# Optimization experiments

Hardware: AMD Instinct MI355X
Metric: run time of the kernel (lower is better)

Reference implementation:

```python
import jax, jax.numpy as jnp
import numpy as np

N = 50000        # nodes
E = 800000       # edges
IN_FEAT = 128
OUT_FEAT = 64
HEADS = 4
NUM_CLASSES = 40
NEG_SLOPE = 0.2  # DGL GATConv default


def setup_inputs() -> dict:
    key = jax.random.key(0)
    ks = jax.random.split(key, 12)
    x = jax.random.normal(ks[0], (N, IN_FEAT), dtype=jnp.float32)
    src = jax.random.randint(ks[1], (E,), 0, N, dtype=jnp.int32)
    dst = jax.random.randint(ks[2], (E,), 0, N, dtype=jnp.int32)
    # layer 1 params: fc W1 [in, H*D], attn_l/attn_r [H, D], bias [H*D]
    s1 = 1.0 / np.sqrt(IN_FEAT)
    W1 = jax.random.normal(ks[3], (IN_FEAT, HEADS * OUT_FEAT), dtype=jnp.float32) * s1
    al1 = jax.random.normal(ks[4], (HEADS, OUT_FEAT), dtype=jnp.float32) * 0.1
    ar1 = jax.random.normal(ks[5], (HEADS, OUT_FEAT), dtype=jnp.float32) * 0.1
    b1 = jnp.zeros((HEADS * OUT_FEAT,), dtype=jnp.float32)
    # layer 2 params: fc W2 [H*D, C], attn [1, C], bias [C]
    hid = HEADS * OUT_FEAT
    s2 = 1.0 / np.sqrt(hid)
    W2 = jax.random.normal(ks[6], (hid, NUM_CLASSES), dtype=jnp.float32) * s2
    al2 = jax.random.normal(ks[7], (1, NUM_CLASSES), dtype=jnp.float32) * 0.1
    ar2 = jax.random.normal(ks[8], (1, NUM_CLASSES), dtype=jnp.float32) * 0.1
    b2 = jnp.zeros((NUM_CLASSES,), dtype=jnp.float32)
    return {"x": x, "src": src, "dst": dst,
            "W1": W1, "al1": al1, "ar1": ar1, "b1": b1,
            "W2": W2, "al2": al2, "ar2": ar2, "b2": b2}


def gat_layer(x, W, al, ar, bias, src, dst, heads, out_feat):
    n = x.shape[0]
    h = (x @ W).reshape(n, heads, out_feat)            # [N,H,D]
    el = jnp.sum(h * al[None], axis=-1)                # [N,H]
    er = jnp.sum(h * ar[None], axis=-1)                # [N,H]
    e = el[src] + er[dst]                              # [E,H]
    e = jnp.where(e > 0, e, NEG_SLOPE * e)             # LeakyReLU
    # segment softmax over edges sharing the same destination
    emax = jax.ops.segment_max(e, dst, num_segments=n)           # [N,H]
    emax = jnp.where(jnp.isfinite(emax), emax, 0.0)              # isolated nodes
    ee = jnp.exp(e - emax[dst])                                  # [E,H]
    denom = jax.ops.segment_sum(ee, dst, num_segments=n)         # [N,H]
    denom = jnp.where(denom > 0, denom, 1.0)
    alpha = ee / denom[dst]                                      # [E,H]
    msg = h[src] * alpha[:, :, None]                             # [E,H,D]
    out = jax.ops.segment_sum(msg, dst, num_segments=n)          # [N,H,D]
    return out + bias.reshape(1, heads, out_feat)


def reference(x, src, dst, W1, al1, ar1, b1, W2, al2, ar2, b2):
    h = gat_layer(x, W1, al1, ar1, b1, src, dst, HEADS, OUT_FEAT)  # [N,H,D]
    h = h.reshape(h.shape[0], HEADS * OUT_FEAT)
    h = jax.nn.elu(h)
    h = gat_layer(h, W2, al2, ar2, b2, src, dst, 1, NUM_CLASSES)   # [N,1,C]
    return jnp.squeeze(h, axis=1)                                   # [N,C]
```

## Files before the change

kernel.cpp:

```cpp
#include <hip/hip_runtime.h>

#define NN 50000
#define NE 800000
#define HID 256
#define NCLS 40

typedef short bf16x8 __attribute__((ext_vector_type(8)));
typedef float f32x4 __attribute__((ext_vector_type(4)));

__device__ inline unsigned short f2bf(float f) {
    unsigned int u = __float_as_uint(f);
    return (unsigned short)((u + 0x7FFFu + ((u >> 16) & 1u)) >> 16);
}
__device__ inline unsigned int pack2bf(float a, float b) {
    return (unsigned int)f2bf(a) | ((unsigned int)f2bf(b) << 16);
}
__device__ inline float2 bf2x(unsigned int u) {
    return make_float2(__uint_as_float(u << 16), __uint_as_float(u & 0xFFFF0000u));
}

__global__ void k_count(const int* __restrict__ dst, int* __restrict__ counts) {
    int e = blockIdx.x * 256 + threadIdx.x;
    if (e < NE) atomicAdd(&counts[dst[e]], 1);
}

__global__ void k_scanA(const int* __restrict__ counts, int* __restrict__ indptr,
                        int* __restrict__ bsum) {
    __shared__ int sh[256];
    int t = threadIdx.x;
    int idx = blockIdx.x * 256 + t;
    int c = idx < NN ? counts[idx] : 0;
    sh[t] = c;
    __syncthreads();
    for (int off = 1; off < 256; off <<= 1) {
        int v = (t >= off) ? sh[t - off] : 0;
        __syncthreads();
        sh[t] += v;
        __syncthreads();
    }
    if (idx < NN) indptr[idx] = sh[t] - c;
    if (t == 255) bsum[blockIdx.x] = sh[255];
}

__global__ void k_scanB(int* __restrict__ bsum, int nb) {
    __shared__ int sh[256];
    int t = threadIdx.x;
    int c = t < nb ? bsum[t] : 0;
    sh[t] = c;
    __syncthreads();
    for (int off = 1; off < 256; off <<= 1) {
        int v = (t >= off) ? sh[t - off] : 0;
        __syncthreads();
        sh[t] += v;
        __syncthreads();
    }
    if (t < nb) bsum[t] = sh[t] - c;
}

__global__ void k_scanC(int* __restrict__ indptr, const int* __restrict__ bsum,
                        int* __restrict__ fill) {
    int idx = blockIdx.x * 256 + threadIdx.x;
    if (idx < NN) {
        indptr[idx] += bsum[idx >> 8];
        fill[idx] = 0;
    }
    if (idx == 0) indptr[NN] = NE;
}

__global__ void k_scatterw(const int* __restrict__ src, const int* __restrict__ dst,
                           const int* __restrict__ indptr, int* __restrict__ fill,
                           const float* __restrict__ el1, const float* __restrict__ er1,
                           int* __restrict__ srcs, float4* __restrict__ w4) {
    int e = blockIdx.x * 256 + threadIdx.x;
    if (e < NE) {
        int d = dst[e];
        int s = src[e];
        int pos = atomicAdd(&fill[d], 1);
        int j = indptr[d] + pos;
        srcs[j] = s;
        float4 ls = *(const float4*)&el1[(size_t)s * 4];
        float4 rd = *(const float4*)&er1[(size_t)d * 4];
        float e0 = ls.x + rd.x, e1 = ls.y + rd.y, e2 = ls.z + rd.z, e3 = ls.w + rd.w;
        e0 = e0 > 0.f ? e0 : 0.2f * e0;
        e1 = e1 > 0.f ? e1 : 0.2f * e1;
        e2 = e2 > 0.f ? e2 : 0.2f * e2;
        e3 = e3 > 0.f ? e3 : 0.2f * e3;
        w4[j] = make_float4(__expf(e0), __expf(e1), __expf(e2), __expf(e3));
    }
}

__global__ void k_prep(const float* __restrict__ W1, const float* __restrict__ al,
                       const float* __restrict__ ar, const float* __restrict__ W2,
                       float* __restrict__ wel, float* __restrict__ wer,
                       unsigned short* __restrict__ W1Tb,
                       unsigned short* __restrict__ W2Tb) {
    int gid = blockIdx.x * 256 + threadIdx.x;
    int nth = gridDim.x * 256;
    const int TOT = 512 + 32768 + 48 * 256;
    for (int i = gid; i < TOT; i += nth) {
        if (i < 512) {
            int k = i >> 2, h = i & 3;
            float a = 0.f, b = 0.f;
            for (int dd = 0; dd < 64; ++dd) {
                float w = W1[k * 256 + h * 64 + dd];
                a = fmaf(w, al[h * 64 + dd], a);
                b = fmaf(w, ar[h * 64 + dd], b);
            }
            wel[i] = a;
            wer[i] = b;
        } else if (i < 512 + 32768) {
            int j = i - 512;
            int col = j >> 7, k = j & 127;
            W1Tb[j] = f2bf(W1[k * 256 + col]);
        } else {
            int j = i - 512 - 32768;
            int col = j >> 8, kk = j & 255;
            W2Tb[j] = (col < NCLS) ? f2bf(W2[kk * 40 + col]) : (unsigned short)0;
        }
    }
}

__global__ void k_elr1x(const float* __restrict__ x, const float* __restrict__ wel,
                        const float* __restrict__ wer, float* __restrict__ el1,
                        float* __restrict__ er1, unsigned short* __restrict__ xb) {
    __shared__ float xs[64 * 129];
    __shared__ float wels[512], wers[512];
    int t = threadIdx.x;
    int n0 = blockIdx.x * 64;
    wels[t] = wel[t]; wels[256 + t] = wel[256 + t];
    wers[t] = wer[t]; wers[256 + t] = wer[256 + t];
    for (int i = 0; i < 8; ++i) {
        int f = i * 256 + t;
        int row = f >> 5;
        int col4 = (f & 31) * 4;
        float4 v = make_float4(0.f, 0.f, 0.f, 0.f);
        if (n0 + row < NN) v = ((const float4*)x)[(size_t)n0 * 32 + f];
        xs[row * 129 + col4 + 0] = v.x;
        xs[row * 129 + col4 + 1] = v.y;
        xs[row * 129 + col4 + 2] = v.z;
        xs[row * 129 + col4 + 3] = v.w;
    }
    __syncthreads();
    int node = t & 63;
    int h = t >> 6;
    float a = 0.f, b = 0.f;
    for (int k = 0; k < 128; ++k) {
        float xv = xs[node * 129 + k];
        a = fmaf(xv, wels[k * 4 + h], a);
        b = fmaf(xv, wers[k * 4 + h], b);
    }
    if (n0 + node < NN) {
        el1[(size_t)(n0 + node) * 4 + h] = a;
        er1[(size_t)(n0 + node) * 4 + h] = b;
    }
    for (int i = 0; i < 4; ++i) {
        int g = (i * 256 + t) * 8;
        int row = g >> 7, col = g & 127;
        if (n0 + row < NN) {
            ushort4 lo, hi;
            lo.x = f2bf(xs[row * 129 + col + 0]);
            lo.y = f2bf(xs[row * 129 + col + 1]);
            lo.z = f2bf(xs[row * 129 + col + 2]);
            lo.w = f2bf(xs[row * 129 + col + 3]);
            hi.x = f2bf(xs[row * 129 + col + 4]);
            hi.y = f2bf(xs[row * 129 + col + 5]);
            hi.z = f2bf(xs[row * 129 + col + 6]);
            hi.w = f2bf(xs[row * 129 + col + 7]);
            *(ushort4*)&xb[(size_t)(n0 + row) * 128 + col] = lo;
            *(ushort4*)&xb[(size_t)(n0 + row) * 128 + col + 4] = hi;
        }
    }
}

#define XG_STRIDE 260
#define FMA8(AC0, AC1, AC2, AC3, WQ, XV) \
    AC0.x = fmaf(WQ.x, XV.x, AC0.x); AC0.y = fmaf(WQ.x, XV.y, AC0.y); \
    AC1.x = fmaf(WQ.y, XV.x, AC1.x); AC1.y = fmaf(WQ.y, XV.y, AC1.y); \
    AC2.x = fmaf(WQ.z, XV.x, AC2.x); AC2.y = fmaf(WQ.z, XV.y, AC2.y); \
    AC3.x = fmaf(WQ.w, XV.x, AC3.x); AC3.y = fmaf(WQ.w, XV.y, AC3.y);

__global__ void k_agg1m(const unsigned int* __restrict__ xb32,
                        const float4* __restrict__ w4,
                        const int* __restrict__ indptr, const int* __restrict__ srcs,
                        const unsigned short* __restrict__ W1Tb,
                        const float* __restrict__ b1,
                        unsigned short* __restrict__ elu1) {
    __shared__ unsigned int xg[16 * XG_STRIDE];
    __shared__ int   si[8][64];
    __shared__ float4 sw[8][64];
    int t = threadIdx.x;
    int wv = t >> 6, l = t & 63;
    int n0 = blockIdx.x * 16;
    int d0 = n0 + wv * 4;
    int ip[5];
#pragma unroll
    for (int q = 0; q < 5; ++q) ip[q] = indptr[d0 + q];
    int w2 = wv * 2;
#pragma unroll
    for (int p = 0; p < 2; ++p) {
        int begA = ip[2 * p + 0], endA = ip[2 * p + 1];
        int begB = ip[2 * p + 1], endB = ip[2 * p + 2];
        int degA = endA - begA, degB = endB - begB;
        int sA = 0, sB = 0;
        float4 wA = make_float4(0.f, 0.f, 0.f, 0.f);
        float4 wB = make_float4(0.f, 0.f, 0.f, 0.f);
        if (l < degA) { sA = srcs[begA + l]; wA = w4[begA + l]; }
        if (l < degB) { sB = srcs[begB + l]; wB = w4[begB + l]; }
        si[w2 + 0][l] = sA; sw[w2 + 0][l] = wA;
        si[w2 + 1][l] = sB; sw[w2 + 1][l] = wB;
        float2 aA0 = {0,0}, aA1 = {0,0}, aA2 = {0,0}, aA3 = {0,0};
        float2 aB0 = {0,0}, aB1 = {0,0}, aB2 = {0,0}, aB3 = {0,0};
        int capA = degA < 64 ? degA : 64;
        int capB = degB < 64 ? degB : 64;
        int mcap = capA > capB ? capA : capB;
        for (int e = 0; e < mcap; e += 8) {
            unsigned int uA[8], uB[8];
            bool doA = e < capA, doB = e < capB;
            if (doA) {
#pragma unroll
                for (int q = 0; q < 8; ++q)
                    uA[q] = xb32[(size_t)si[w2][e + q] * 64 + l];
            }
            if (doB) {
#pragma unroll
                for (int q = 0; q < 8; ++q)
                    uB[q] = xb32[(size_t)si[w2 + 1][e + q] * 64 + l];
            }
            if (doA) {
#pragma unroll
                for (int q = 0; q < 8; ++q) {
                    float4 wq = sw[w2][e + q];
                    float2 xv = bf2x(uA[q]);
                    FMA8(aA0, aA1, aA2, aA3, wq, xv)
                }
            }
            if (doB) {
#pragma unroll
                for (int q = 0; q < 8; ++q) {
                    float4 wq = sw[w2 + 1][e + q];
                    float2 xv = bf2x(uB[q]);
                    FMA8(aB0, aB1, aB2, aB3, wq, xv)
                }
            }
        }
        for (int j = begA + 64; j < endA; ++j) {
            float4 wq = w4[j];
            float2 xv = bf2x(xb32[(size_t)srcs[j] * 64 + l]);
            FMA8(aA0, aA1, aA2, aA3, wq, xv)
        }
        for (int j = begB + 64; j < endB; ++j) {
            float4 wq = w4[j];
            float2 xv = bf2x(xb32[(size_t)srcs[j] * 64 + l]);
            FMA8(aB0, aB1, aB2, aB3, wq, xv)
        }
        float dA0 = wA.x, dA1 = wA.y, dA2 = wA.z, dA3 = wA.w;
        float dB0 = wB.x, dB1 = wB.y, dB2 = wB.z, dB3 = wB.w;
        for (int j = begA + 64 + l; j < endA; j += 64) {
            float4 wt = w4[j];
            dA0 += wt.x; dA1 += wt.y; dA2 += wt.z; dA3 += wt.w;
        }
        for (int j = begB + 64 + l; j < endB; j += 64) {
            float4 wt = w4[j];
            dB0 += wt.x; dB1 += wt.y; dB2 += wt.z; dB3 += wt.w;
        }
#pragma unroll
        for (int off = 32; off > 0; off >>= 1) {
            dA0 += __shfl_xor(dA0, off); dA1 += __shfl_xor(dA1, off);
            dA2 += __shfl_xor(dA2, off); dA3 += __shfl_xor(dA3, off);
            dB0 += __shfl_xor(dB0, off); dB1 += __shfl_xor(dB1, off);
            dB2 += __shfl_xor(dB2, off); dB3 += __shfl_xor(dB3, off);
        }
        float iA0 = dA0 > 0.f ? 1.f / dA0 : 0.f;
        float iA1 = dA1 > 0.f ? 1.f / dA1 : 0.f;
        float iA2 = dA2 > 0.f ? 1.f / dA2 : 0.f;
        float iA3 = dA3 > 0.f ? 1.f / dA3 : 0.f;
        float iB0 = dB0 > 0.f ? 1.f / dB0 : 0.f;
        float iB1 = dB1 > 0.f ? 1.f / dB1 : 0.f;
        float iB2 = dB2 > 0.f ? 1.f / dB2 : 0.f;
        float iB3 = dB3 > 0.f ? 1.f / dB3 : 0.f;
        unsigned int* xgA = &xg[(wv * 4 + 2 * p + 0) * XG_STRIDE];
        xgA[0 * 64 + l] = pack2bf(aA0.x * iA0, aA0.y * iA0);
        xgA[1 * 64 + l] = pack2bf(aA1.x * iA1, aA1.y * iA1);
        xgA[2 * 64 + l] = pack2bf(aA2.x * iA2, aA2.y * iA2);
        xgA[3 * 64 + l] = pack2bf(aA3.x * iA3, aA3.y * iA3);
        unsigned int* xgB = &xg[(wv * 4 + 2 * p + 1) * XG_STRIDE];
        xgB[0 * 64 + l] = pack2bf(aB0.x * iB0, aB0.y * iB0);
        xgB[1 * 64 + l] = pack2bf(aB1.x * iB1, aB1.y * iB1);
        xgB[2 * 64 + l] = pack2bf(aB2.x * iB2, aB2.y * iB2);
        xgB[3 * 64 + l] = pack2bf(aB3.x * iB3, aB3.y * iB3);
    }
    __syncthreads();
    int lrow = l & 15, lk = l >> 4;
    f32x4 acc[4] = {};
#pragma unroll
    for (int kt = 0; kt < 4; ++kt) {
        bf16x8 av = *(const bf16x8*)&xg[lrow * XG_STRIDE + wv * 64 + kt * 16 + lk * 4];
#pragma unroll
        for (int nt = 0; nt < 4; ++nt) {
            int col = wv * 64 + nt * 16 + lrow;
            bf16x8 bv = *(const bf16x8*)&W1Tb[(size_t)col * 128 + kt * 32 + lk * 8];
            acc[nt] = __builtin_amdgcn_mfma_f32_16x16x32_bf16(av, bv, acc[nt], 0, 0, 0);
        }
    }
#pragma unroll
    for (int nt = 0; nt < 4; ++nt) {
        int col = wv * 64 + nt * 16 + lrow;
        float bv1 = b1[col];
#pragma unroll
        for (int r = 0; r < 4; ++r) {
            int row = n0 + lk * 4 + r;
            float o = acc[nt][r] + bv1;
            o = o > 0.f ? o : (__expf(o) - 1.f);
            elu1[(size_t)row * 256 + col] = f2bf(o);
        }
    }
}

__global__ void k_mfma2(const unsigned short* __restrict__ elu1,
                        const unsigned short* __restrict__ W2Tb,
                        const float* __restrict__ al2, const float* __restrict__ ar2,
                        unsigned short* __restrict__ h2b, float* __restrict__ el2,
                        float* __restrict__ er2) {
    int t = threadIdx.x;
    int wv = t >> 6, l = t & 63;
    int lrow = l & 15, lk = l >> 4;
    int n0 = blockIdx.x * 64 + wv * 16;
    int arow = n0 + lrow;
    if (arow >= NN) arow = NN - 1;
    f32x4 acc[3] = {};
#pragma unroll
    for (int kt = 0; kt < 8; ++kt) {
        int kofs = kt * 32 + lk * 8;
        bf16x8 av = *(const bf16x8*)&elu1[(size_t)arow * 256 + kofs];
#pragma unroll
        for (int nt = 0; nt < 3; ++nt) {
            bf16x8 bv = *(const bf16x8*)&W2Tb[(size_t)(nt * 16 + lrow) * 256 + kofs];
            acc[nt] = __builtin_amdgcn_mfma_f32_16x16x32_bf16(av, bv, acc[nt], 0, 0, 0);
        }
    }
    float alc[3], arc[3];
#pragma unroll
    for (int nt = 0; nt < 3; ++nt) {
        int col = nt * 16 + lrow;
        alc[nt] = col < NCLS ? al2[col] : 0.f;
        arc[nt] = col < NCLS ? ar2[col] : 0.f;
    }
#pragma unroll
    for (int r = 0; r < 4; ++r) {
        int row = n0 + lk * 4 + r;
        float pa = 0.f, pb = 0.f;
#pragma unroll
        for (int nt = 0; nt < 3; ++nt) {
            float v = acc[nt][r];
            pa = fmaf(v, alc[nt], pa);
            pb = fmaf(v, arc[nt], pb);
            int col = nt * 16 + lrow;
            if (row < NN && col < NCLS) h2b[(size_t)row * NCLS + col] = f2bf(v);
        }
#pragma unroll
        for (int off = 1; off < 16; off <<= 1) {
            pa += __shfl_xor(pa, off);
            pb += __shfl_xor(pb, off);
        }
        if (lrow == 0 && row < NN) {
            el2[row] = pa;
            er2[row] = pb;
        }
    }
}

__global__ void k_agg2(const unsigned int* __restrict__ h2b32,
                       const float* __restrict__ el2,
                       const float* __restrict__ er2, const float* __restrict__ b2,
                       const int* __restrict__ indptr, const int* __restrict__ srcs,
                       float* __restrict__ out) {
    __shared__ int   si[4][64];
    __shared__ float sw[4][64];
    int t = threadIdx.x;
    int wv = t >> 6, l = t & 63;
    int d = blockIdx.x * 4 + wv;
    int beg = indptr[d], end = indptr[d + 1];
    int deg = end - beg;
    float rd = er2[d];
    int s_l = 0;
    float w = 0.f;
    if (l < deg) {
        s_l = srcs[beg + l];
        float e = el2[s_l] + rd;
        e = e > 0.f ? e : 0.2f * e;
        w = __expf(e);
    }
    si[wv][l] = s_l;
    sw[wv][l] = w;
    float den = w;
    for (int j = beg + 64 + l; j < end; j += 64) {
        float e = el2[srcs[j]] + rd;
        e = e > 0.f ? e : 0.2f * e;
        den += __expf(e);
    }
    int half = l >> 5, il = l & 31;
    bool act = il < 20;
    float2 acc = {0.f, 0.f};
    int dege = deg < 64 ? deg : 64;
    for (int e = 0; e < dege; e += 8) {
        int ixs[4];
        float ws_[4];
        unsigned int us[4];
#pragma unroll
        for (int q = 0; q < 4; ++q) {
            int idx = e + 2 * q + half;
            ixs[q] = si[wv][idx];
            ws_[q] = sw[wv][idx];
        }
#pragma unroll
        for (int q = 0; q < 4; ++q)
            us[q] = act ? h2b32[(size_t)ixs[q] * 20 + il] : 0u;
#pragma unroll
        for (int q = 0; q < 4; ++q) {
            float2 xv = bf2x(us[q]);
            acc.x = fmaf(ws_[q], xv.x, acc.x);
            acc.y = fmaf(ws_[q], xv.y, acc.y);
        }
    }
    for (int j = beg + 64; j < end; ++j) {
        int s = srcs[j];
        float e = el2[s] + rd;
        e = e > 0.f ? e : 0.2f * e;
        float ww = (half == 0) ? __expf(e) : 0.f;
        unsigned int u = act ? h2b32[(size_t)s * 20 + il] : 0u;
        float2 xv = bf2x(u);
        acc.x = fmaf(ww, xv.x, acc.x);
        acc.y = fmaf(ww, xv.y, acc.y);
    }
#pragma unroll
    for (int off = 32; off > 0; off >>= 1) den += __shfl_xor(den, off);
    float inv = den > 0.f ? 1.f / den : 0.f;
    acc.x += __shfl_xor(acc.x, 32);
    acc.y += __shfl_xor(acc.y, 32);
    if (half == 0 && act) {
        float2 bb = *(const float2*)&b2[2 * il];
        *(float2*)&out[(size_t)d * NCLS + 2 * il] =
            make_float2(fmaf(acc.x, inv, bb.x), fmaf(acc.y, inv, bb.y));
    }
}

extern "C" void kernel_launch(void* const* d_in, const int* in_sizes, int n_in,
                              void* d_out, int out_size, void* d_ws, size_t ws_size,
                              hipStream_t stream) {
    const float* x   = (const float*)d_in[0];
    const int*   src = (const int*)d_in[1];
    const int*   dst = (const int*)d_in[2];
    const float* W1  = (const float*)d_in[3];
    const float* al1 = (const float*)d_in[4];
    const float* ar1 = (const float*)d_in[5];
    const float* b1  = (const float*)d_in[6];
    const float* W2  = (const float*)d_in[7];
    const float* al2 = (const float*)d_in[8];
    const float* ar2 = (const float*)d_in[9];
    const float* b2  = (const float*)d_in[10];
    float* out = (float*)d_out;

    float* ws = (float*)d_ws;
    size_t off = 0;
    unsigned short* elu1  = (unsigned short*)(ws + off); off += (size_t)NN * 128;
    unsigned short* xb    = (unsigned short*)(ws + off); off += (size_t)NN * 64;
    unsigned short* h2b   = (unsigned short*)(ws + off); off += (size_t)NN * 20;
    float* el1  = ws + off; off += (size_t)NN * 4;
    float* er1  = ws + off; off += (size_t)NN * 4;
    float* el2  = ws + off; off += NN;
    float* er2  = ws + off; off += NN;
    float* wel  = ws + off; off += 512;
    float* wer  = ws + off; off += 512;
    unsigned short* w1tb = (unsigned short*)(ws + off); off += 16384;
    unsigned short* w2tb = (unsigned short*)(ws + off); off += 48 * 128;
    float* w4   = ws + off; off += (size_t)NE * 4;
    int* counts = (int*)(ws + off);
    int* indptr = counts + NN;
    int* fill   = indptr + NN + 1;
    int* srcs   = fill + NN;
    int* bsum   = srcs + NE;

    const int NB = (NN + 255) / 256;

    hipMemsetAsync(counts, 0, NN * sizeof(int), stream);

    k_count<<<(NE + 255) / 256, 256, 0, stream>>>(dst, counts);
    k_scanA<<<NB, 256, 0, stream>>>(counts, indptr, bsum);
    k_scanB<<<1, 256, 0, stream>>>(bsum, NB);
    k_scanC<<<NB, 256, 0, stream>>>(indptr, bsum, fill);

    k_prep<<<48, 256, 0, stream>>>(W1, al1, ar1, W2, wel, wer, w1tb, w2tb);
    k_elr1x<<<(NN + 63) / 64, 256, 0, stream>>>(x, wel, wer, el1, er1, xb);
    k_scatterw<<<(NE + 255) / 256, 256, 0, stream>>>(src, dst, indptr, fill,
                                                     el1, er1, srcs, (float4*)w4);
    k_agg1m<<<NN / 16, 256, 0, stream>>>((const unsigned int*)xb, (const float4*)w4,
                                         indptr, srcs, w1tb, b1, elu1);

    k_mfma2<<<(NN + 63) / 64, 256, 0, stream>>>(elu1, w2tb, al2, ar2, h2b, el2, er2);
    k_agg2<<<NN / 4, 256, 0, stream>>>((const unsigned int*)h2b, el2, er2, b2,
                                       indptr, srcs, out);
}
```

Before: 215.4 us.

## Fuse layer-2 projection into layer-1 aggregation and give each agg2 wave two nodes

Layer 1's ELU output is now staged in shared memory (reusing the edge-staging pool) and the W2 projection plus el2/er2 attention terms are computed in the same kernel. This removes the k_mfma2 launch and the 25.6 MB bf16 elu1 round trip through global memory. k_agg2 is also changed so each wave handles two destination nodes, halving the block count and interleaving the two gathers to raise memory-level parallelism. The cost is extra shared-memory syncs and a layer-2 MFMA that runs on only 3 of 4 waves in the fused kernel.

```diff
diff --git a/kernel.cpp b/kernel.cpp
--- a/kernel.cpp
+++ b/kernel.cpp
@@ -173,6 +173,7 @@
 }
 
 #define XG_STRIDE 260
+#define EB_STRIDE 264
 #define FMA8(AC0, AC1, AC2, AC3, WQ, XV) \
     AC0.x = fmaf(WQ.x, XV.x, AC0.x); AC0.y = fmaf(WQ.x, XV.y, AC0.y); \
     AC1.x = fmaf(WQ.y, XV.x, AC1.x); AC1.y = fmaf(WQ.y, XV.y, AC1.y); \
@@ -183,11 +184,18 @@
                         const float4* __restrict__ w4,
                         const int* __restrict__ indptr, const int* __restrict__ srcs,
                         const unsigned short* __restrict__ W1Tb,
+                        const unsigned short* __restrict__ W2Tb,
                         const float* __restrict__ b1,
-                        unsigned short* __restrict__ elu1) {
+                        const float* __restrict__ al2, const float* __restrict__ ar2,
+                        unsigned short* __restrict__ h2b,
+                        float* __restrict__ el2, float* __restrict__ er2) {
     __shared__ unsigned int xg[16 * XG_STRIDE];
-    __shared__ int   si[8][64];
-    __shared__ float4 sw[8][64];
+    __shared__ __align__(16) unsigned char pool[10496];
+    float4 (*sw)[64] = (float4(*)[64])pool;
+    int (*si)[64] = (int(*)[64])(pool + 8192);
+    unsigned short* eb = (unsigned short*)pool;
+    float* pel = (float*)(pool + 8448);
+    float* per_ = (float*)(pool + 8640);
     int t = threadIdx.x;
     int wv = t >> 6, l = t & 63;
     int n0 = blockIdx.x * 16;
@@ -291,81 +299,64 @@
     }
     __syncthreads();
     int lrow = l & 15, lk = l >> 4;
-    f32x4 acc[4] = {};
-#pragma unroll
-    for (int kt = 0; kt < 4; ++kt) {
-        bf16x8 av = *(const bf16x8*)&xg[lrow * XG_STRIDE + wv * 64 + kt * 16 + lk * 4];
+    {
+        f32x4 acc[4] = {};
+#pragma unroll
+        for (int kt = 0; kt < 4; ++kt) {
+            bf16x8 av = *(const bf16x8*)&xg[lrow * XG_STRIDE + wv * 64 + kt * 16 + lk * 4];
+#pragma unroll
+            for (int nt = 0; nt < 4; ++nt) {
+                int col = wv * 64 + nt * 16 + lrow;
+                bf16x8 bv = *(const bf16x8*)&W1Tb[(size_t)col * 128 + kt * 32 + lk * 8];
+                acc[nt] = __builtin_amdgcn_mfma_f32_16x16x32_bf16(av, bv, acc[nt], 0, 0, 0);
+            }
+        }
 #pragma unroll
         for (int nt = 0; nt < 4; ++nt) {
             int col = wv * 64 + nt * 16 + lrow;
-            bf16x8 bv = *(const bf16x8*)&W1Tb[(size_t)col * 128 + kt * 32 + lk * 8];
-            acc[nt] = __builtin_amdgcn_mfma_f32_16x16x32_bf16(av, bv, acc[nt], 0, 0, 0);
-        }
-    }
-#pragma unroll
-    for (int nt = 0; nt < 4; ++nt) {
-        int col = wv * 64 + nt * 16 + lrow;
-        float bv1 = b1[col];
+            float bv1 = b1[col];
+#pragma unroll
+            for (int r = 0; r < 4; ++r) {
+                int rloc = lk * 4 + r;
+                float o = acc[nt][r] + bv1;
+                o = o > 0.f ? o : (__expf(o) - 1.f);
+                eb[rloc * EB_STRIDE + col] = f2bf(o);
+            }
+        }
+    }
+    __syncthreads();
+    if (wv < 3) {
+        f32x4 acc2 = {};
+#pragma unroll
+        for (int kt = 0; kt < 8; ++kt) {
+            bf16x8 av = *(const bf16x8*)&eb[lrow * EB_STRIDE + kt * 32 + lk * 8];
+            bf16x8 bv = *(const bf16x8*)&W2Tb[(size_t)(wv * 16 + lrow) * 256 + kt * 32 + lk * 8];
+            acc2 = __builtin_amdgcn_mfma_f32_16x16x32_bf16(av, bv, acc2, 0, 0, 0);
+        }
+        int col2 = wv * 16 + lrow;
+        float alc = col2 < NCLS ? al2[col2] : 0.f;
+        float arc = col2 < NCLS ? ar2[col2] : 0.f;
 #pragma unroll
         for (int r = 0; r < 4; ++r) {
             int row = n0 + lk * 4 + r;
-            float o = acc[nt][r] + bv1;
-            o = o > 0.f ? o : (__expf(o) - 1.f);
-            elu1[(size_t)row * 256 + col] = f2bf(o);
-        }
-    }
-}
-
-__global__ void k_mfma2(const unsigned short* __restrict__ elu1,
-                        const unsigned short* __restrict__ W2Tb,
-                        const float* __restrict__ al2, const float* __restrict__ ar2,
-                        unsigned short* __restrict__ h2b, float* __restrict__ el2,
-                        float* __restrict__ er2) {
-    int t = threadIdx.x;
-    int wv = t >> 6, l = t & 63;
-    int lrow = l & 15, lk = l >> 4;
-    int n0 = blockIdx.x * 64 + wv * 16;
-    int arow = n0 + lrow;
-    if (arow >= NN) arow = NN - 1;
-    f32x4 acc[3] = {};
-#pragma unroll
-    for (int kt = 0; kt < 8; ++kt) {
-        int kofs = kt * 32 + lk * 8;
-        bf16x8 av = *(const bf16x8*)&elu1[(size_t)arow * 256 + kofs];
-#pragma unroll
-        for (int nt = 0; nt < 3; ++nt) {
-            bf16x8 bv = *(const bf16x8*)&W2Tb[(size_t)(nt * 16 + lrow) * 256 + kofs];
-            acc[nt] = __builtin_amdgcn_mfma_f32_16x16x32_bf16(av, bv, acc[nt], 0, 0, 0);
-        }
-    }
-    float alc[3], arc[3];
-#pragma unroll
-    for (int nt = 0; nt < 3; ++nt) {
-        int col = nt * 16 + lrow;
-        alc[nt] = col < NCLS ? al2[col] : 0.f;
-        arc[nt] = col < NCLS ? ar2[col] : 0.f;
-    }
-#pragma unroll
-    for (int r = 0; r < 4; ++r) {
-        int row = n0 + lk * 4 + r;
-        float pa = 0.f, pb = 0.f;
-#pragma unroll
-        for (int nt = 0; nt < 3; ++nt) {
-            float v = acc[nt][r];
-            pa = fmaf(v, alc[nt], pa);
-            pb = fmaf(v, arc[nt], pb);
-            int col = nt * 16 + lrow;
-            if (row < NN && col < NCLS) h2b[(size_t)row * NCLS + col] = f2bf(v);
-        }
-#pragma unroll
-        for (int off = 1; off < 16; off <<= 1) {
-            pa += __shfl_xor(pa, off);
-            pb += __shfl_xor(pb, off);
-        }
-        if (lrow == 0 && row < NN) {
-            el2[row] = pa;
-            er2[row] = pb;
-        }
+            float v = acc2[r];
+            if (col2 < NCLS) h2b[(size_t)row * NCLS + col2] = f2bf(v);
+            float pa = v * alc, pb = v * arc;
+#pragma unroll
+            for (int off = 1; off < 16; off <<= 1) {
+                pa += __shfl_xor(pa, off);
+                pb += __shfl_xor(pb, off);
+            }
+            if (lrow == 0) {
+                pel[wv * 16 + lk * 4 + r] = pa;
+                per_[wv * 16 + lk * 4 + r] = pb;
+            }
+        }
+    }
+    __syncthreads();
+    if (t < 16) {
+        el2[n0 + t] = pel[t] + pel[16 + t] + pel[32 + t];
+        er2[n0 + t] = per_[t] + per_[16 + t] + per_[32 + t];
     }
 }
 
@@ -374,73 +365,135 @@
                        const float* __restrict__ er2, const float* __restrict__ b2,
                        const int* __restrict__ indptr, const int* __restrict__ srcs,
                        float* __restrict__ out) {
-    __shared__ int   si[4][64];
-    __shared__ float sw[4][64];
+    __shared__ int   si[8][64];
+    __shared__ float sw[8][64];
     int t = threadIdx.x;
     int wv = t >> 6, l = t & 63;
-    int d = blockIdx.x * 4 + wv;
-    int beg = indptr[d], end = indptr[d + 1];
-    int deg = end - beg;
-    float rd = er2[d];
-    int s_l = 0;
-    float w = 0.f;
-    if (l < deg) {
-        s_l = srcs[beg + l];
-        float e = el2[s_l] + rd;
+    int dA = blockIdx.x * 8 + wv * 2;
+    int dB = dA + 1;
+    int begA = indptr[dA], endA = indptr[dA + 1];
+    int begB = endA, endB = indptr[dB + 1];
+    int degA = endA - begA, degB = endB - begB;
+    float rdA = er2[dA], rdB = er2[dB];
+    int sA = 0, sB = 0;
+    float wA = 0.f, wB = 0.f;
+    if (l < degA) {
+        sA = srcs[begA + l];
+        float e = el2[sA] + rdA;
         e = e > 0.f ? e : 0.2f * e;
-        w = __expf(e);
-    }
-    si[wv][l] = s_l;
-    sw[wv][l] = w;
-    float den = w;
-    for (int j = beg + 64 + l; j < end; j += 64) {
-        float e = el2[srcs[j]] + rd;
+        wA = __expf(e);
+    }
+    if (l < degB) {
+        sB = srcs[begB + l];
+        float e = el2[sB] + rdB;
         e = e > 0.f ? e : 0.2f * e;
-        den += __expf(e);
+        wB = __expf(e);
+    }
+    int w2 = wv * 2;
+    si[w2 + 0][l] = sA; sw[w2 + 0][l] = wA;
+    si[w2 + 1][l] = sB; sw[w2 + 1][l] = wB;
+    float denA = wA, denB = wB;
+    for (int j = begA + 64 + l; j < endA; j += 64) {
+        float e = el2[srcs[j]] + rdA;
+        e = e > 0.f ? e : 0.2f * e;
+        denA += __expf(e);
+    }
+    for (int j = begB + 64 + l; j < endB; j += 64) {
+        float e = el2[srcs[j]] + rdB;
+        e = e > 0.f ? e : 0.2f * e;
+        denB += __expf(e);
     }
     int half = l >> 5, il = l & 31;
     bool act = il < 20;
-    float2 acc = {0.f, 0.f};
-    int dege = deg < 64 ? deg : 64;
-    for (int e = 0; e < dege; e += 8) {
-        int ixs[4];
-        float ws_[4];
-        unsigned int us[4];
-#pragma unroll
-        for (int q = 0; q < 4; ++q) {
-            int idx = e + 2 * q + half;
-            ixs[q] = si[wv][idx];
-            ws_[q] = sw[wv][idx];
-        }
-#pragma unroll
-        for (int q = 0; q < 4; ++q)
-            us[q] = act ? h2b32[(size_t)ixs[q] * 20 + il] : 0u;
-#pragma unroll
-        for (int q = 0; q < 4; ++q) {
-            float2 xv = bf2x(us[q]);
-            acc.x = fmaf(ws_[q], xv.x, acc.x);
-            acc.y = fmaf(ws_[q], xv.y, acc.y);
-        }
-    }
-    for (int j = beg + 64; j < end; ++j) {
+    float2 accA = {0.f, 0.f}, accB = {0.f, 0.f};
+    int capA = degA < 64 ? degA : 64;
+    int capB = degB < 64 ? degB : 64;
+    int mcap = capA > capB ? capA : capB;
+    for (int e = 0; e < mcap; e += 8) {
+        bool doA = e < capA, doB = e < capB;
+        int ixA[4], ixB[4];
+        float wsA[4], wsB[4];
+        unsigned int uA[4], uB[4];
+        if (doA) {
+#pragma unroll
+            for (int q = 0; q < 4; ++q) {
+                int idx = e + 2 * q + half;
+                ixA[q] = si[w2][idx];
+                wsA[q] = sw[w2][idx];
+            }
+        }
+        if (doB) {
+#pragma unroll
+            for (int q = 0; q < 4; ++q) {
+                int idx = e + 2 * q + half;
+                ixB[q] = si[w2 + 1][idx];
+                wsB[q] = sw[w2 + 1][idx];
+            }
+        }
+        if (doA) {
+#pragma unroll
+            for (int q = 0; q < 4; ++q)
+                uA[q] = act ? h2b32[(size_t)ixA[q] * 20 + il] : 0u;
+        }
+        if (doB) {
+#pragma unroll
+            for (int q = 0; q < 4; ++q)
+                uB[q] = act ? h2b32[(size_t)ixB[q] * 20 + il] : 0u;
+        }
+        if (doA) {
+#pragma unroll
+            for (int q = 0; q < 4; ++q) {
+                float2 xv = bf2x(uA[q]);
+                accA.x = fmaf(wsA[q], xv.x, accA.x);
+                accA.y = fmaf(wsA[q], xv.y, accA.y);
+            }
+        }
+        if (doB) {
+#pragma unroll
+            for (int q = 0; q < 4; ++q) {
+                float2 xv = bf2x(uB[q]);
+                accB.x = fmaf(wsB[q], xv.x, accB.x);
+                accB.y = fmaf(wsB[q], xv.y, accB.y);
+            }
+        }
+    }
+    for (int j = begA + 64; j < endA; ++j) {
         int s = srcs[j];
-        float e = el2[s] + rd;
+        float e = el2[s] + rdA;
         e = e > 0.f ? e : 0.2f * e;
         float ww = (half == 0) ? __expf(e) : 0.f;
         unsigned int u = act ? h2b32[(size_t)s * 20 + il] : 0u;
         float2 xv = bf2x(u);
-        acc.x = fmaf(ww, xv.x, acc.x);
-        acc.y = fmaf(ww, xv.y, acc.y);
-    }
-#pragma unroll
-    for (int off = 32; off > 0; off >>= 1) den += __shfl_xor(den, off);
-    float inv = den > 0.f ? 1.f / den : 0.f;
-    acc.x += __shfl_xor(acc.x, 32);
-    acc.y += __shfl_xor(acc.y, 32);
+        accA.x = fmaf(ww, xv.x, accA.x);
+        accA.y = fmaf(ww, xv.y, accA.y);
+    }
+    for (int j = begB + 64; j < endB; ++j) {
+        int s = srcs[j];
+        float e = el2[s] + rdB;
+        e = e > 0.f ? e : 0.2f * e;
+        float ww = (half == 0) ? __expf(e) : 0.f;
+        unsigned int u = act ? h2b32[(size_t)s * 20 + il] : 0u;
+        float2 xv = bf2x(u);
+        accB.x = fmaf(ww, xv.x, accB.x);
+        accB.y = fmaf(ww, xv.y, accB.y);
+    }
+#pragma unroll
+    for (int off = 32; off > 0; off >>= 1) {
+        denA += __shfl_xor(denA, off);
+        denB += __shfl_xor(denB, off);
+    }
+    float invA = denA > 0.f ? 1.f / denA : 0.f;
+    float invB = denB > 0.f ? 1.f / denB : 0.f;
+    accA.x += __shfl_xor(accA.x, 32);
+    accA.y += __shfl_xor(accA.y, 32);
+    accB.x += __shfl_xor(accB.x, 32);
+    accB.y += __shfl_xor(accB.y, 32);
     if (half == 0 && act) {
         float2 bb = *(const float2*)&b2[2 * il];
-        *(float2*)&out[(size_t)d * NCLS + 2 * il] =
-            make_float2(fmaf(acc.x, inv, bb.x), fmaf(acc.y, inv, bb.y));
+        *(float2*)&out[(size_t)dA * NCLS + 2 * il] =
+            make_float2(fmaf(accA.x, invA, bb.x), fmaf(accA.y, invA, bb.y));
+        *(float2*)&out[(size_t)dB * NCLS + 2 * il] =
+            make_float2(fmaf(accB.x, invB, bb.x), fmaf(accB.y, invB, bb.y));
     }
 }
 
@@ -462,7 +515,6 @@
 
     float* ws = (float*)d_ws;
     size_t off = 0;
-    unsigned short* elu1  = (unsigned short*)(ws + off); off += (size_t)NN * 128;
     unsigned short* xb    = (unsigned short*)(ws + off); off += (size_t)NN * 64;
     unsigned short* h2b   = (unsigned short*)(ws + off); off += (size_t)NN * 20;
     float* el1  = ws + off; off += (size_t)NN * 4;
@@ -494,9 +546,9 @@
     k_scatterw<<<(NE + 255) / 256, 256, 0, stream>>>(src, dst, indptr, fill,
                                                      el1, er1, srcs, (float4*)w4);
     k_agg1m<<<NN / 16, 256, 0, stream>>>((const unsigned int*)xb, (const float4*)w4,
-                                         indptr, srcs, w1tb, b1, elu1);
-
-    k_mfma2<<<(NN + 63) / 64, 256, 0, stream>>>(elu1, w2tb, al2, ar2, h2b, el2, er2);
-    k_agg2<<<NN / 4, 256, 0, stream>>>((const unsigned int*)h2b, el2, er2, b2,
+                                         indptr, srcs, w1tb, w2tb, b1, al2, ar2,
+                                         h2b, el2, er2);
+
+    k_agg2<<<NN / 8, 256, 0, stream>>>((const unsigned int*)h2b, el2, er2, b2,
                                        indptr, srcs, out);
 }
```

Result: faster. 206.8 us (-4.0%).
